# Kernel optimization log

Hardware: AMD Instinct MI355X
Metric: run time of the kernel (lower is better)

The kernel has to match this reference:

```python
import jax, jax.numpy as jnp
import numpy as np

# Cyclic permutation matrices applied after each flow step (dimension==3 branch)
P_XY = jnp.array([[0, 1, 0], [1, 0, 0], [0, 0, 1]], dtype=jnp.float32)
P_XZ = jnp.array([[0, 0, 1], [0, 1, 0], [1, 0, 0]], dtype=jnp.float32)
P_YZ = jnp.array([[0, 1, 0], [0, 0, 1], [1, 0, 0]], dtype=jnp.float32)

N = 1_000_000   # number of atoms / samples
FLOW_DEPTH = 8


def setup_inputs() -> dict:
    key = jax.random.key(0)
    k1, k2, k3 = jax.random.split(key, 3)
    z = jax.random.normal(k1, (N, 3), dtype=jnp.float32)
    w = jax.random.normal(k2, (N, FLOW_DEPTH, 3, 3), dtype=jnp.float32)
    b = jax.random.normal(k3, (N, FLOW_DEPTH, 3), dtype=jnp.float32)
    return {"z": z, "w": w, "b": b}


def _flow_zx(z, w, b):
    # z: [N,3], w: [N,D,3,3], b: [N,D,3]
    eye = jnp.eye(3, dtype=w.dtype)
    diag = jnp.diagonal(w, axis1=-2, axis2=-1)               # [N,D,3]
    # LU parameterization: unit lower-tri L, positive diag D, unit upper-tri U
    l = jnp.tril(w, -1) + eye
    u = jnp.triu(w, 1) + eye
    # Faithful to original: log-det uses |0.1 + diag|, D uses |diag| + 0.1
    d_log_det = jnp.sum(jnp.log(jnp.abs(0.1 + diag)), axis=(1, 2))  # [N]
    du = (jnp.abs(diag) + 0.1)[..., :, None] * u             # D @ U, [N,D,3,3]
    W = jnp.einsum('ndij,ndjk->ndik', l, du)                  # L @ D @ U
    perms = [P_XY, P_YZ, P_XZ]
    depth = w.shape[1]
    for idx in range(depth):  # static, small flow depth
        z = jnp.einsum('nb,nbd->nd', z, W[:, idx]) + b[:, idx]
        z = z @ perms[idx % 3]
    return z, d_log_det


def reference(z, w, b):
    return _flow_zx(z, w, b)
```

## Files before the change

### kernel.cpp

```cpp
#include <hip/hip_runtime.h>

#define FLOW_DEPTH 8

__global__ __launch_bounds__(256) void graphflow_kernel(
    const float* __restrict__ z_in,
    const float* __restrict__ w,
    const float* __restrict__ b,
    float* __restrict__ out,
    int n_atoms)
{
    int n = blockIdx.x * blockDim.x + threadIdx.x;
    if (n >= n_atoms) return;

    float z0 = z_in[n * 3 + 0];
    float z1 = z_in[n * 3 + 1];
    float z2 = z_in[n * 3 + 2];

    const float4* w4 = reinterpret_cast<const float4*>(w) + (size_t)n * 18;
    float4 wv[18];
#pragma unroll
    for (int i = 0; i < 18; ++i) wv[i] = w4[i];

    const float4* b4 = reinterpret_cast<const float4*>(b) + (size_t)n * 6;
    float4 bv[6];
#pragma unroll
    for (int i = 0; i < 6; ++i) bv[i] = b4[i];

    const float* wf = reinterpret_cast<const float*>(wv);
    const float* bf = reinterpret_cast<const float*>(bv);

    float logdet = 0.0f;

#pragma unroll
    for (int d = 0; d < FLOW_DEPTH; ++d) {
        const float* W = wf + d * 9;
        float w00 = W[0], w01 = W[1], w02 = W[2];
        float w10 = W[3], w11 = W[4], w12 = W[5];
        float w20 = W[6], w21 = W[7], w22 = W[8];

        float d0 = fabsf(w00) + 0.1f;
        float d1 = fabsf(w11) + 0.1f;
        float d2 = fabsf(w22) + 0.1f;
        logdet += logf(fabsf(0.1f + w00)) +
                  logf(fabsf(0.1f + w11)) +
                  logf(fabsf(0.1f + w22));

        float m01 = d0 * w01;
        float m02 = d0 * w02;
        float m12 = d1 * w12;
        float M00 = d0;
        float M01 = m01;
        float M02 = m02;
        float M10 = w10 * d0;
        float M11 = fmaf(w10, m01, d1);
        float M12 = fmaf(w10, m02, m12);
        float M20 = w20 * d0;
        float M21 = fmaf(w20, m01, w21 * d1);
        float M22 = fmaf(w20, m02, fmaf(w21, m12, d2));

        float t0 = fmaf(z0, M00, fmaf(z1, M10, fmaf(z2, M20, bf[d * 3 + 0])));
        float t1 = fmaf(z0, M01, fmaf(z1, M11, fmaf(z2, M21, bf[d * 3 + 1])));
        float t2 = fmaf(z0, M02, fmaf(z1, M12, fmaf(z2, M22, bf[d * 3 + 2])));

        int p = d % 3;
        if (p == 0) {
            z0 = t1; z1 = t0; z2 = t2;
        } else if (p == 1) {
            z0 = t2; z1 = t0; z2 = t1;
        } else {
            z0 = t2; z1 = t1; z2 = t0;
        }
    }

    out[n * 3 + 0] = z0;
    out[n * 3 + 1] = z1;
    out[n * 3 + 2] = z2;
    out[(size_t)3 * n_atoms + n] = logdet;
}

extern "C" void kernel_launch(void* const* d_in, const int* in_sizes, int n_in,
                              void* d_out, int out_size, void* d_ws, size_t ws_size,
                              hipStream_t stream) {
    const float* z = (const float*)d_in[0];
    const float* w = (const float*)d_in[1];
    const float* b = (const float*)d_in[2];
    float* out = (float*)d_out;

    int n_atoms = in_sizes[0] / 3;
    const int block = 256;
    int grid = (n_atoms + block - 1) / block;

    hipLaunchKernelGGL(graphflow_kernel, dim3(grid), dim3(block), 0, stream,
                       z, w, b, out, n_atoms);
}
```

Before: 471.7 us.

## Stage per-atom weights through LDS with coalesced global_load_lds transfers

New measurement: 447.7 us. 5.1% less time.

```diff
diff --git a/kernel.cpp b/kernel.cpp
--- a/kernel.cpp
+++ b/kernel.cpp
@@ -1,33 +1,72 @@
 #include <hip/hip_runtime.h>
 
 #define FLOW_DEPTH 8
+#define BLOCK 64
+#define W_F4 18
+#define B_F4 6
 
-__global__ __launch_bounds__(256) void graphflow_kernel(
+typedef const __attribute__((address_space(1))) void g_void;
+typedef __attribute__((address_space(3))) void l_void;
+
+__global__ __launch_bounds__(BLOCK) void graphflow_kernel(
     const float* __restrict__ z_in,
     const float* __restrict__ w,
     const float* __restrict__ b,
     float* __restrict__ out,
     int n_atoms)
 {
-    int n = blockIdx.x * blockDim.x + threadIdx.x;
+    __shared__ float4 sw[BLOCK * W_F4];
+    __shared__ float4 sb[BLOCK * B_F4];
+
+    const int t = threadIdx.x;
+    const int atom0 = blockIdx.x * BLOCK;
+
+    const float4* gw = reinterpret_cast<const float4*>(w) + (size_t)atom0 * W_F4;
+    const float4* gb = reinterpret_cast<const float4*>(b) + (size_t)atom0 * B_F4;
+
+    if (atom0 + BLOCK <= n_atoms) {
+#pragma unroll
+        for (int k = 0; k < W_F4; ++k) {
+            __builtin_amdgcn_global_load_lds((g_void*)(gw + k * BLOCK + t),
+                                             (l_void*)(sw + k * BLOCK), 16, 0, 0);
+        }
+#pragma unroll
+        for (int k = 0; k < B_F4; ++k) {
+            __builtin_amdgcn_global_load_lds((g_void*)(gb + k * BLOCK + t),
+                                             (l_void*)(sb + k * BLOCK), 16, 0, 0);
+        }
+    } else {
+        int nw = (n_atoms - atom0) * W_F4;
+        for (int k = 0; k < W_F4; ++k) {
+            int idx = k * BLOCK + t;
+            if (idx < nw) sw[idx] = gw[idx];
+        }
+        int nb = (n_atoms - atom0) * B_F4;
+        for (int k = 0; k < B_F4; ++k) {
+            int idx = k * BLOCK + t;
+            if (idx < nb) sb[idx] = gb[idx];
+        }
+    }
+
+    __builtin_amdgcn_s_waitcnt(0);
+    __syncthreads();
+
+    const int n = atom0 + t;
     if (n >= n_atoms) return;
+
+    float4 wr[W_F4];
+#pragma unroll
+    for (int j = 0; j < W_F4; ++j) wr[j] = sw[t * W_F4 + j];
+    float4 br[B_F4];
+#pragma unroll
+    for (int j = 0; j < B_F4; ++j) br[j] = sb[t * B_F4 + j];
+
+    const float* wf = reinterpret_cast<const float*>(wr);
+    const float* bf = reinterpret_cast<const float*>(br);
 
     float z0 = z_in[n * 3 + 0];
     float z1 = z_in[n * 3 + 1];
     float z2 = z_in[n * 3 + 2];
-
-    const float4* w4 = reinterpret_cast<const float4*>(w) + (size_t)n * 18;
-    float4 wv[18];
-#pragma unroll
-    for (int i = 0; i < 18; ++i) wv[i] = w4[i];
-
-    const float4* b4 = reinterpret_cast<const float4*>(b) + (size_t)n * 6;
-    float4 bv[6];
-#pragma unroll
-    for (int i = 0; i < 6; ++i) bv[i] = b4[i];
-
-    const float* wf = reinterpret_cast<const float*>(wv);
-    const float* bf = reinterpret_cast<const float*>(bv);
 
     float logdet = 0.0f;
 
@@ -87,9 +126,8 @@
     float* out = (float*)d_out;
 
     int n_atoms = in_sizes[0] / 3;
-    const int block = 256;
-    int grid = (n_atoms + block - 1) / block;
+    int grid = (n_atoms + BLOCK - 1) / BLOCK;
 
-    hipLaunchKernelGGL(graphflow_kernel, dim3(grid), dim3(block), 0, stream,
+    hipLaunchKernelGGL(graphflow_kernel, dim3(grid), dim3(BLOCK), 0, stream,
                        z, w, b, out, n_atoms);
 }
```
